# Optimization experiments

Hardware: AMD Instinct MI355X
Metric: run time of the kernel (lower is better)

Reference implementation:

```python
import jax, jax.numpy as jnp
import numpy as np

B, T, C = 64, 256, 1024
H, DH = 16, 64           # n_heads, head_dim (C == H*DH)
NP, WS = 16, 2           # n_patches per side, window_size (T == NP*NP)
EPS = 1e-5


def setup_inputs() -> dict:
    key = jax.random.key(0)
    ks = jax.random.split(key, 8)
    s = lambda k, shape, fan: jax.random.normal(k, shape, jnp.float32) * (fan ** -0.5)
    return dict(
        x=jax.random.normal(ks[0], (B, T, C), jnp.float32),
        ln1_g=jnp.ones((C,), jnp.float32), ln1_b=jnp.zeros((C,), jnp.float32),
        Wq=s(ks[1], (H, C, DH), C), Wk=s(ks[2], (H, C, DH), C), Wv=s(ks[3], (H, C, DH), C),
        Wp=s(ks[4], (C, C), C), bp=jnp.zeros((C,), jnp.float32),
        ln2_g=jnp.ones((C,), jnp.float32), ln2_b=jnp.zeros((C,), jnp.float32),
        W1=s(ks[5], (C, C), C), b1=jnp.zeros((C,), jnp.float32),
        W2=s(ks[6], (C, C), C), b2=jnp.zeros((C,), jnp.float32))


def _ln(x, g, b):
    m = x.mean(-1, keepdims=True)
    v = x.var(-1, keepdims=True)
    return (x - m) * jax.lax.rsqrt(v + EPS) * g + b


def reference(x, ln1_g, ln1_b, Wq, Wk, Wv, Wp, bp, ln2_g, ln2_b, W1, b1, W2, b2):
    h = NP // WS                      # windows per side = 8
    nw = h * h                        # 64 windows of WS*WS = 4 tokens
    xn = _ln(x, ln1_g, ln1_b)
    # window partition: [B, T, C] -> [B*nw, WS*WS, C]
    xw = (xn.reshape(B, h, WS, h, WS, C)
            .transpose(0, 1, 3, 2, 4, 5)
            .reshape(B * nw, WS * WS, C))
    # all-heads batched QKV (original loops over heads; math identical since
    # torch.cat of per-head outputs == head-axis stack then reshape)
    q = jnp.einsum('ntc,hcd->nhtd', xw, Wq)
    k = jnp.einsum('ntc,hcd->nhtd', xw, Wk)
    v = jnp.einsum('ntc,hcd->nhtd', xw, Wv)
    # NOTE: scale is C**-0.5 with C = d_model (faithful to source, not head_dim)
    wei = jax.nn.softmax(jnp.einsum('nhqd,nhkd->nhqk', q, k) * (C ** -0.5), axis=-1)
    att = jnp.einsum('nhqk,nhkd->nhqd', wei, v)
    att = att.transpose(0, 2, 1, 3).reshape(B * nw, WS * WS, C)
    att = att @ Wp + bp
    # residual adds the LayerNorm-ed, window-partitioned x (faithful quirk)
    xr = xw + att
    # reverse window partition -> [B, T, C]
    xr = (xr.reshape(B, h, h, WS, WS, C)
            .transpose(0, 1, 3, 2, 4, 5)
            .reshape(B, T, C))
    ff = jax.nn.gelu(_ln(xr, ln2_g, ln2_b) @ W1 + b1, approximate=False) @ W2 + b2
    return xr + ff
```

## Files before the change

kernel.cpp:

```cpp
#include <hip/hip_runtime.h>
#include <math.h>

typedef unsigned short u16;
typedef unsigned int   u32;

using f32x4  = __attribute__((ext_vector_type(4))) float;
using s16x8  = __attribute__((ext_vector_type(8))) short;
using u16x8  = __attribute__((ext_vector_type(8))) unsigned short;

__device__ __forceinline__ u16 f2b(float f) {
    u32 u = __float_as_uint(f);
    u += 0x7FFFu + ((u >> 16) & 1u);
    return (u16)(u >> 16);
}
__device__ __forceinline__ float b2f(u16 u) { return __uint_as_float(((u32)u) << 16); }

__device__ __forceinline__ int natrow(int R) {
    int b = R >> 8, r8 = R & 255, w = r8 >> 2, t = r8 & 3;
    return (b << 8) + ((((w >> 3) << 1) + (t >> 1)) << 4) + ((w & 7) << 1) + (t & 1);
}

__device__ __forceinline__ void gll16(const void* g, void* l) {
    __builtin_amdgcn_global_load_lds(
        (const __attribute__((address_space(1))) void*)g,
        (__attribute__((address_space(3))) void*)l, 16, 0, 0);
}

__global__ __launch_bounds__(256) void prologue_kernel(
    const float* __restrict__ x, const float* __restrict__ ln1g, const float* __restrict__ ln1b,
    const float* __restrict__ Wq, const float* __restrict__ Wk, const float* __restrict__ Wv,
    const float* __restrict__ Wp, const float* __restrict__ W1, const float* __restrict__ W2,
    u16* __restrict__ WqkvT, u16* __restrict__ WpT, u16* __restrict__ xw_b)
{
    const int bid = blockIdx.x;
    const int tid = threadIdx.x;
    if (bid < 6144) {
        __shared__ float tile[32][33];
        const float* in; u16* out; int Rr, Cc, bx, by;
        if (bid < 3072) {
            const int z = bid >> 6, r = bid & 63;
            bx = r & 1; by = r >> 1;
            in  = (z < 16 ? Wq : z < 32 ? Wk : Wv) + (size_t)(z & 15) * 65536;
            const int h = z & 15, sec = z < 16 ? 0 : (z < 32 ? 1 : 2);
            out = WqkvT + ((size_t)h * 192 + sec * 64) * 1024;
            Rr = 1024; Cc = 64;
        } else {
            const int t = bid - 3072, z = t >> 10, r = t & 1023;
            bx = r & 31; by = r >> 5;
            in  = z == 0 ? Wp : z == 1 ? W1 : W2;
            out = WpT + (size_t)z * 1048576;
            Rr = 1024; Cc = 1024;
        }
        const int tx = tid & 31, ty = tid >> 5;
        const int c  = bx * 32 + tx;
        const int r0 = by * 32;
#pragma unroll
        for (int i = 0; i < 32; i += 8) tile[ty + i][tx] = in[(size_t)(r0 + ty + i) * Cc + c];
        __syncthreads();
        const int orow0 = bx * 32;
        const int ocol  = r0 + tx;
#pragma unroll
        for (int i = 0; i < 32; i += 8)
            out[(size_t)(orow0 + ty + i) * Rr + ocol] = f2b(tile[tx][ty + i]);
    } else {
        __shared__ float red[8];
        const int R   = bid - 6144;
        const int src = natrow(R);
        const float4 v = ((const float4*)(x + (size_t)src * 1024))[tid];
        float s  = v.x + v.y + v.z + v.w;
        float s2 = v.x * v.x + v.y * v.y + v.z * v.z + v.w * v.w;
#pragma unroll
        for (int o = 32; o; o >>= 1) { s += __shfl_xor(s, o); s2 += __shfl_xor(s2, o); }
        const int w = tid >> 6, l = tid & 63;
        if (l == 0) { red[w] = s; red[w + 4] = s2; }
        __syncthreads();
        s  = red[0] + red[1] + red[2] + red[3];
        s2 = red[4] + red[5] + red[6] + red[7];
        const float mean = s * (1.f / 1024.f);
        const float var  = s2 * (1.f / 1024.f) - mean * mean;
        const float rinv = rsqrtf(var + 1e-5f);
        const float4 gv = ((const float4*)ln1g)[tid];
        const float4 bv = ((const float4*)ln1b)[tid];
        ((ushort4*)(xw_b + (size_t)R * 1024))[tid] = make_ushort4(
            f2b((v.x - mean) * rinv * gv.x + bv.x), f2b((v.y - mean) * rinv * gv.y + bv.y),
            f2b((v.z - mean) * rinv * gv.z + bv.z), f2b((v.w - mean) * rinv * gv.w + bv.w));
    }
}

__global__ __launch_bounds__(256) void ln2_kernel(
    const u16* __restrict__ X, const float* __restrict__ g, const float* __restrict__ bta,
    u16* __restrict__ outB)
{
    const int R = blockIdx.x;
    const ushort4 r = ((const ushort4*)(X + (size_t)R * 1024))[threadIdx.x];
    const float x0 = b2f(r.x), x1 = b2f(r.y), x2 = b2f(r.z), x3 = b2f(r.w);
    float s  = x0 + x1 + x2 + x3;
    float s2 = x0 * x0 + x1 * x1 + x2 * x2 + x3 * x3;
#pragma unroll
    for (int o = 32; o; o >>= 1) { s += __shfl_xor(s, o); s2 += __shfl_xor(s2, o); }
    __shared__ float red[8];
    const int w = threadIdx.x >> 6, l = threadIdx.x & 63;
    if (l == 0) { red[w] = s; red[w + 4] = s2; }
    __syncthreads();
    s  = red[0] + red[1] + red[2] + red[3];
    s2 = red[4] + red[5] + red[6] + red[7];
    const float mean = s * (1.f / 1024.f);
    const float var  = s2 * (1.f / 1024.f) - mean * mean;
    const float rinv = rsqrtf(var + 1e-5f);
    const float4 gv = ((const float4*)g)[threadIdx.x];
    const float4 bv = ((const float4*)bta)[threadIdx.x];
    ((ushort4*)(outB + (size_t)R * 1024))[threadIdx.x] = make_ushort4(
        f2b((x0 - mean) * rinv * gv.x + bv.x), f2b((x1 - mean) * rinv * gv.y + bv.y),
        f2b((x2 - mean) * rinv * gv.z + bv.z), f2b((x3 - mean) * rinv * gv.w + bv.w));
}

__global__ __launch_bounds__(512, 2) void gemm_qkv_attn(
    const u16* __restrict__ A, const u16* __restrict__ Bt,
    u16* __restrict__ Att, int M, int K)
{
    extern __shared__ char lds[];
    const int NT = K >> 6;
    const int x = blockIdx.x & 7, i = blockIdx.x >> 3;
    const int sc = i >> 4, u = i & 15;
    const int scr = sc >> 2, scc = sc & 3;
    const int mb = x * 8 + scr * 4 + (u >> 2);
    const int nb = scc * 4 + (u & 3);
    const int row0 = mb * 256, col0 = nb * 192;
    const int tid = threadIdx.x;
    const int w = tid >> 6, l = tid & 63;
    const int wr = w & 3, wcg = w >> 2;
    const int lr = l & 15, kg = l >> 4;
    const int xs = (lr & 7) << 4;
    const int koff[2] = { (kg * 16) ^ xs, (64 + kg * 16) ^ xs };
    const int abase_l = wr * 8192 + lr * 128;
    const int bbase_l = wcg * 12288 + lr * 128;

    f32x4 acc[4][6] = {};
    s16x8 a[4][2], b[6][2];

    auto stageQ = [&](int ts) {
        if (ts >= NT) return;
        const int d = ts & 1, gcolb = ts * 64;
        const int sl = (tid & 7) ^ ((tid >> 3) & 7);
#pragma unroll
        for (int h2 = 0; h2 < 2; ++h2)
#pragma unroll
            for (int j = 0; j < 2; ++j) {
                const int c = j * 512 + tid;
                const int s2 = (c & 7) ^ ((c >> 3) & 7);
                gll16(A + (size_t)(row0 + h2 * 128 + (c >> 3)) * K + gcolb + s2 * 8,
                      lds + d * 32768 + h2 * 16384 + (j * 8 + w) * 1024);
            }
#pragma unroll
        for (int k2 = 0; k2 < 3; ++k2)
            gll16(Bt + (size_t)(col0 + k2 * 64 + (tid >> 3)) * K + gcolb + sl * 8,
                  lds + 65536 + d * 24576 + k2 * 8192 + w * 1024);
    };

#define SB __builtin_amdgcn_sched_barrier(0)
#define WLq(NS) do { asm volatile("s_waitcnt lgkmcnt(" NS ")" ::: "memory"); SB; } while (0)

    stageQ(0);

    for (int t = 0; t < NT; ++t) {
        const char* Ab = lds + (t & 1) * 32768 + abase_l;
        const char* Bb = lds + 65536 + (t & 1) * 24576 + bbase_l;
        asm volatile("s_waitcnt vmcnt(0)" ::: "memory");
        __builtin_amdgcn_s_barrier(); SB;
#pragma unroll
        for (int i2 = 0; i2 < 4; ++i2) a[i2][0] = *(const s16x8*)(Ab + i2 * 2048 + koff[0]);
#pragma unroll
        for (int n = 0; n < 6; ++n)   b[n][0]  = *(const s16x8*)(Bb + n * 2048 + koff[0]);
        SB;
#pragma unroll
        for (int i2 = 0; i2 < 4; ++i2) a[i2][1] = *(const s16x8*)(Ab + i2 * 2048 + koff[1]);
#pragma unroll
        for (int n = 0; n < 6; ++n)   b[n][1]  = *(const s16x8*)(Bb + n * 2048 + koff[1]);
        SB;
        stageQ(t + 1); SB;
        __builtin_amdgcn_s_setprio(1);
        WLq("10");
#pragma unroll
        for (int i2 = 0; i2 < 4; ++i2)
#pragma unroll
            for (int n = 0; n < 6; ++n)
                acc[i2][n] = __builtin_amdgcn_mfma_f32_16x16x32_bf16(a[i2][0], b[n][0], acc[i2][n], 0, 0, 0);
        SB;
        WLq("0");
#pragma unroll
        for (int i2 = 0; i2 < 4; ++i2)
#pragma unroll
            for (int n = 0; n < 6; ++n)
                acc[i2][n] = __builtin_amdgcn_mfma_f32_16x16x32_bf16(a[i2][1], b[n][1], acc[i2][n], 0, 0, 0);
        __builtin_amdgcn_s_setprio(0); SB;
    }
#undef WLq

    __builtin_amdgcn_s_barrier();
    u16* attL = (u16*)lds;
#pragma unroll
    for (int i2 = 0; i2 < 4; ++i2)
#pragma unroll
        for (int n = 0; n < 6; ++n)
#pragma unroll
            for (int j = 0; j < 4; ++j)
                attL[(wr * 64 + i2 * 16 + kg * 4 + j) * 200 + wcg * 96 + n * 16 + lr] =
                    f2b(acc[i2][n][j]);
    __builtin_amdgcn_s_barrier();

    {
        const int wl = tid >> 3, j = tid & 7;
        const float scale = 0.03125f;
        u16x8 qv[4], kv[4], vv[4];
#pragma unroll
        for (int t = 0; t < 4; ++t) {
            qv[t] = *(const u16x8*)&attL[(wl * 4 + t) * 200 + j * 8];
            kv[t] = *(const u16x8*)&attL[(wl * 4 + t) * 200 + 64 + j * 8];
            vv[t] = *(const u16x8*)&attL[(wl * 4 + t) * 200 + 128 + j * 8];
        }
        float qf[4][8], kf[4][8];
#pragma unroll
        for (int t = 0; t < 4; ++t)
#pragma unroll
            for (int c = 0; c < 8; ++c) { qf[t][c] = b2f(qv[t][c]); kf[t][c] = b2f(kv[t][c]); }
        float s[4][4];
#pragma unroll
        for (int t = 0; t < 4; ++t)
#pragma unroll
            for (int u2 = 0; u2 < 4; ++u2) {
                float p = qf[t][0] * kf[u2][0];
#pragma unroll
                for (int c = 1; c < 8; ++c) p += qf[t][c] * kf[u2][c];
                p += __shfl_xor(p, 1); p += __shfl_xor(p, 2); p += __shfl_xor(p, 4);
                s[t][u2] = p * scale;
            }
#pragma unroll
        for (int t = 0; t < 4; ++t) {
            const float m = fmaxf(fmaxf(s[t][0], s[t][1]), fmaxf(s[t][2], s[t][3]));
            const float e0 = expf(s[t][0] - m), e1 = expf(s[t][1] - m);
            const float e2 = expf(s[t][2] - m), e3 = expf(s[t][3] - m);
            const float inv = 1.f / (e0 + e1 + e2 + e3);
            u16x8 o;
#pragma unroll
            for (int c = 0; c < 8; ++c)
                o[c] = f2b((e0 * b2f(vv[0][c]) + e1 * b2f(vv[1][c]) +
                            e2 * b2f(vv[2][c]) + e3 * b2f(vv[3][c])) * inv);
            *(u16x8*)(Att + (size_t)(row0 + wl * 4 + t) * 1024 + nb * 64 + j * 8) = o;
        }
    }
#undef SB
}

template<int MODE>
__global__ __launch_bounds__(512, 2) void gemm256(
    const u16* __restrict__ A, const u16* __restrict__ Bt,
    const float* __restrict__ bias, const void* __restrict__ resid,
    void* __restrict__ Out, int M, int N, int K, int LDA, int NB)
{
    extern __shared__ char lds[];
    const int NT = K >> 6;
    const int nblk = gridDim.x;
    const int x = blockIdx.x & 7, i = blockIdx.x >> 3;
    const int R = (nblk >> 3) / NB;
    const int ncs = NB >> 2;
    const int sc = i >> 4, u = i & 15;
    const int scr = sc / ncs, scc = sc - scr * ncs;
    const int mb = x * R + scr * 4 + (u >> 2);
    const int nb = scc * 4 + (u & 3);
    const int row0 = mb * 256, col0 = nb * 256;
    const int tid = threadIdx.x;
    const int w = tid >> 6, l = tid & 63;
    const int wr = w >> 2, wc = w & 3;
    const int lr = l & 15, kg = l >> 4;
    const int xs = (lr & 7) << 4;
    const int koff[2] = { (kg * 16) ^ xs, (64 + kg * 16) ^ xs };
    const int abase_l = wr * 8192 + lr * 128;
    const int bbase_l = wc * 4096 + lr * 128;

    f32x4 acc[2][2][4][2] = {};
    s16x8 a0[4][2], a1[4][2], b0[2][2], b1[2][2];

    auto stage = [&](int ts, int item) {
        if (ts >= NT) return;
        const int d = ts & 1;
        const int isB = item & 1, h = item >> 1;
        char* lbase = lds + (isB ? 65536 : 0) + d * 32768 + h * 16384;
        const u16* gptr = isB ? Bt : A;
        const int ld = isB ? K : LDA;
        const int blk0 = (isB ? col0 : row0) + h * 128;
#pragma unroll
        for (int j = 0; j < 2; ++j) {
            const int p = j * 512 + tid;
            const int q = p ^ ((p >> 3) & 7);
            gll16(gptr + (size_t)(blk0 + (q >> 3)) * ld + ts * 64 + (q & 7) * 8,
                  lbase + (j * 8 + w) * 1024);
        }
    };

#define SB __builtin_amdgcn_sched_barrier(0)
#define LOAD_A(dst, qm) do { \
    _Pragma("unroll") for (int kk = 0; kk < 2; ++kk) \
    _Pragma("unroll") for (int i2 = 0; i2 < 4; ++i2) \
        dst[i2][kk] = *(const s16x8*)(Ab + (qm) * 16384 + abase_l + i2 * 2048 + koff[kk]); \
} while (0)
#define LOAD_B(dst, qn) do { \
    _Pragma("unroll") for (int kk = 0; kk < 2; ++kk) \
    _Pragma("unroll") for (int n = 0; n < 2; ++n) \
        dst[n][kk] = *(const s16x8*)(Bb + (qn) * 16384 + bbase_l + n * 2048 + koff[kk]); \
} while (0)
#define LGKM0 do { asm volatile("s_waitcnt lgkmcnt(0)" ::: "memory"); SB; } while (0)
#define MFMA_Q(qm, qn, aa, bb) do { \
    __builtin_amdgcn_s_setprio(1); \
    _Pragma("unroll") for (int kk = 0; kk < 2; ++kk) \
    _Pragma("unroll") for (int i2 = 0; i2 < 4; ++i2) \
    _Pragma("unroll") for (int n = 0; n < 2; ++n) \
        acc[qm][qn][i2][n] = __builtin_amdgcn_mfma_f32_16x16x32_bf16( \
            aa[i2][kk], bb[n][kk], acc[qm][qn][i2][n], 0, 0, 0); \
    __builtin_amdgcn_s_setprio(0); SB; \
} while (0)
#define GATE(NSTR) do { \
    asm volatile("s_waitcnt vmcnt(" NSTR ")" ::: "memory"); \
    __builtin_amdgcn_s_barrier(); SB; \
} while (0)

    stage(0, 0); stage(0, 1); stage(0, 2); stage(0, 3);

    for (int t = 0; t < NT - 1; ++t) {
        const char* Ab = lds + (t & 1) * 32768;
        const char* Bb = lds + 65536 + (t & 1) * 32768;
        GATE("4");
        LOAD_A(a0, 0); LOAD_B(b0, 0); SB;
        stage(t + 1, 0); SB;
        LGKM0;
        MFMA_Q(0, 0, a0, b0);
        GATE("4");
        LOAD_A(a1, 1); SB;
        stage(t + 1, 1); SB;
        LGKM0;
        MFMA_Q(1, 0, a1, b0);
        GATE("4");
        LOAD_B(b1, 1); SB;
        stage(t + 1, 2); SB;
        LGKM0;
        MFMA_Q(1, 1, a1, b1);
        stage(t + 1, 3); SB;
        MFMA_Q(0, 1, a0, b1);
    }
    {
        const int t = NT - 1;
        const char* Ab = lds + (t & 1) * 32768;
        const char* Bb = lds + 65536 + (t & 1) * 32768;
        GATE("4");
        LOAD_A(a0, 0); LOAD_B(b0, 0); SB;
        LGKM0;
        MFMA_Q(0, 0, a0, b0);
        GATE("2");
        LOAD_A(a1, 1); SB;
        LGKM0;
        MFMA_Q(1, 0, a1, b0);
        GATE("0");
        LOAD_B(b1, 1); SB;
        LGKM0;
        MFMA_Q(1, 1, a1, b1);
        MFMA_Q(0, 1, a0, b1);
    }
#undef SB
#undef LOAD_A
#undef LOAD_B
#undef LGKM0
#undef MFMA_Q
#undef GATE

#pragma unroll
    for (int qm = 0; qm < 2; ++qm)
#pragma unroll
    for (int i2 = 0; i2 < 4; ++i2) {
        const int grb = row0 + qm * 128 + wr * 64 + i2 * 16 + kg * 4;
#pragma unroll
        for (int qn = 0; qn < 2; ++qn)
#pragma unroll
        for (int n = 0; n < 2; ++n) {
            const int gc = col0 + qn * 128 + wc * 32 + n * 16 + lr;
#pragma unroll
            for (int j = 0; j < 4; ++j) {
                const int gr = grb + j;
                const float v = acc[qm][qn][i2][n][j];
                if (MODE == 2) {
                    const float tt = v + bias[gc];
                    ((u16*)Out)[(size_t)gr * N + gc] = f2b(0.5f * tt * (1.f + erff(tt * 0.70710678118f)));
                } else if (MODE == 3) {
                    ((float*)Out)[(size_t)natrow(gr) * N + gc] =
                        v + bias[gc] + b2f(((const u16*)resid)[(size_t)gr * N + gc]);
                } else {
                    ((u16*)Out)[(size_t)gr * N + gc] =
                        f2b(v + bias[gc] + b2f(((const u16*)resid)[(size_t)gr * N + gc]));
                }
            }
        }
    }
}

extern "C" void kernel_launch(void* const* d_in, const int* in_sizes, int n_in,
                              void* d_out, int out_size, void* d_ws, size_t ws_size,
                              hipStream_t stream)
{
    const float* x    = (const float*)d_in[0];
    const float* ln1g = (const float*)d_in[1];
    const float* ln1b = (const float*)d_in[2];
    const float* Wq   = (const float*)d_in[3];
    const float* Wk   = (const float*)d_in[4];
    const float* Wv   = (const float*)d_in[5];
    const float* Wp   = (const float*)d_in[6];
    const float* bp   = (const float*)d_in[7];
    const float* ln2g = (const float*)d_in[8];
    const float* ln2b = (const float*)d_in[9];
    const float* W1   = (const float*)d_in[10];
    const float* b1   = (const float*)d_in[11];
    const float* W2   = (const float*)d_in[12];
    const float* b2   = (const float*)d_in[13];
    float* out = (float*)d_out;

    char* ws = (char*)d_ws;
    const size_t MB = 1024 * 1024;
    u16* xr_b  = (u16*)ws;
    u16* xw_b  = (u16*)(ws + 32 * MB);
    u16* att   = (u16*)(ws + 64 * MB);
    u16* h1b   = (u16*)(ws + 96 * MB);
    u16* ln2bf = (u16*)(ws + 128 * MB);
    u16* WqkvT = (u16*)(ws + 192 * MB);
    u16* WpT   = (u16*)(ws + 198 * MB);
    u16* W1T   = WpT + (1u << 20);
    u16* W2T   = W1T + (1u << 20);

    (void)hipFuncSetAttribute((const void*)gemm_qkv_attn, hipFuncAttributeMaxDynamicSharedMemorySize, 114688);
    (void)hipFuncSetAttribute((const void*)gemm256<2>, hipFuncAttributeMaxDynamicSharedMemorySize, 131072);
    (void)hipFuncSetAttribute((const void*)gemm256<3>, hipFuncAttributeMaxDynamicSharedMemorySize, 131072);
    (void)hipFuncSetAttribute((const void*)gemm256<5>, hipFuncAttributeMaxDynamicSharedMemorySize, 131072);

    const int M = 16384, K = 1024;

    prologue_kernel<<<22528, 256, 0, stream>>>(x, ln1g, ln1b, Wq, Wk, Wv,
                                               Wp, W1, W2, WqkvT, WpT, xw_b);

    gemm_qkv_attn<<<1024, 512, 114688, stream>>>(xw_b, WqkvT, att, M, K);

    gemm256<5><<<256, 512, 131072, stream>>>(att, WpT, bp, xw_b, xr_b, M, 1024, K, K, 4);

    ln2_kernel<<<16384, 256, 0, stream>>>(xr_b, ln2g, ln2b, ln2bf);

    gemm256<2><<<256, 512, 131072, stream>>>(ln2bf, W1T, b1, nullptr, h1b, M, 1024, K, K, 4);

    gemm256<3><<<256, 512, 131072, stream>>>(h1b, W2T, b2, xr_b, out, M, 1024, K, K, 4);
}
```

Measured before the change: 285.6 us.

## Fold LN2 into W1 GEMM via row stats from projection epilogue

Removes the standalone LN2 kernel and its bf16 normalized buffer. The projection GEMM epilogue now accumulates per-row sum and sum-of-squares with atomics. The FC1 GEMM reads the un-normalized residual and applies the mean/rstd correction in its epilogue, with gamma folded into W1 and precomputed column vectors (gamma·W1, beta·W1+b1) built in the prologue. This adds a memset, atomics and some precision risk from the E[x^2]-mean^2 variance and the bf16 rounding of gamma-scaled weights.

Measured after the change: 304.5 us. 1.07x slower.

```diff
diff --git a/kernel.cpp b/kernel.cpp
--- a/kernel.cpp
+++ b/kernel.cpp
@@ -30,39 +30,44 @@
     const float* __restrict__ x, const float* __restrict__ ln1g, const float* __restrict__ ln1b,
     const float* __restrict__ Wq, const float* __restrict__ Wk, const float* __restrict__ Wv,
     const float* __restrict__ Wp, const float* __restrict__ W1, const float* __restrict__ W2,
-    u16* __restrict__ WqkvT, u16* __restrict__ WpT, u16* __restrict__ xw_b)
+    const float* __restrict__ ln2g, const float* __restrict__ ln2b, const float* __restrict__ b1,
+    u16* __restrict__ WqkvT, u16* __restrict__ WpT, u16* __restrict__ xw_b,
+    float* __restrict__ cvec, float* __restrict__ dvp)
 {
     const int bid = blockIdx.x;
     const int tid = threadIdx.x;
     if (bid < 6144) {
         __shared__ float tile[32][33];
-        const float* in; u16* out; int Rr, Cc, bx, by;
+        const float* in; u16* out; int Cc, bx, by, gfold = 0;
         if (bid < 3072) {
             const int z = bid >> 6, r = bid & 63;
             bx = r & 1; by = r >> 1;
             in  = (z < 16 ? Wq : z < 32 ? Wk : Wv) + (size_t)(z & 15) * 65536;
             const int h = z & 15, sec = z < 16 ? 0 : (z < 32 ? 1 : 2);
             out = WqkvT + ((size_t)h * 192 + sec * 64) * 1024;
-            Rr = 1024; Cc = 64;
+            Cc = 64;
         } else {
             const int t = bid - 3072, z = t >> 10, r = t & 1023;
             bx = r & 31; by = r >> 5;
             in  = z == 0 ? Wp : z == 1 ? W1 : W2;
             out = WpT + (size_t)z * 1048576;
-            Rr = 1024; Cc = 1024;
+            Cc = 1024; gfold = (z == 1);
         }
         const int tx = tid & 31, ty = tid >> 5;
         const int c  = bx * 32 + tx;
         const int r0 = by * 32;
 #pragma unroll
-        for (int i = 0; i < 32; i += 8) tile[ty + i][tx] = in[(size_t)(r0 + ty + i) * Cc + c];
+        for (int i = 0; i < 32; i += 8) {
+            const float gs = gfold ? ln2g[r0 + ty + i] : 1.f;
+            tile[ty + i][tx] = in[(size_t)(r0 + ty + i) * Cc + c] * gs;
+        }
         __syncthreads();
         const int orow0 = bx * 32;
         const int ocol  = r0 + tx;
 #pragma unroll
         for (int i = 0; i < 32; i += 8)
-            out[(size_t)(orow0 + ty + i) * Rr + ocol] = f2b(tile[tx][ty + i]);
-    } else {
+            out[(size_t)(orow0 + ty + i) * 1024 + ocol] = f2b(tile[tx][ty + i]);
+    } else if (bid < 22528) {
         __shared__ float red[8];
         const int R   = bid - 6144;
         const int src = natrow(R);
@@ -84,34 +89,27 @@
         ((ushort4*)(xw_b + (size_t)R * 1024))[tid] = make_ushort4(
             f2b((v.x - mean) * rinv * gv.x + bv.x), f2b((v.y - mean) * rinv * gv.y + bv.y),
             f2b((v.z - mean) * rinv * gv.z + bv.z), f2b((v.w - mean) * rinv * gv.w + bv.w));
+    } else {
+        const int kb = bid - 22528;
+        const int n0 = tid * 4;
+        float pc[4] = {0, 0, 0, 0}, pd[4] = {0, 0, 0, 0};
+        for (int r = 0; r < 16; ++r) {
+            const int k = kb * 16 + r;
+            const float gk = ln2g[k], bk = ln2b[k];
+            const float4 wv = *(const float4*)&W1[(size_t)k * 1024 + n0];
+            pc[0] += gk * wv.x; pc[1] += gk * wv.y; pc[2] += gk * wv.z; pc[3] += gk * wv.w;
+            pd[0] += bk * wv.x; pd[1] += bk * wv.y; pd[2] += bk * wv.z; pd[3] += bk * wv.w;
+        }
+        if (kb == 0) {
+            const float4 bb = *(const float4*)&b1[n0];
+            pd[0] += bb.x; pd[1] += bb.y; pd[2] += bb.z; pd[3] += bb.w;
+        }
+#pragma unroll
+        for (int c = 0; c < 4; ++c) {
+            atomicAdd(&cvec[n0 + c], pc[c]);
+            atomicAdd(&dvp[n0 + c], pd[c]);
+        }
     }
-}
-
-__global__ __launch_bounds__(256) void ln2_kernel(
-    const u16* __restrict__ X, const float* __restrict__ g, const float* __restrict__ bta,
-    u16* __restrict__ outB)
-{
-    const int R = blockIdx.x;
-    const ushort4 r = ((const ushort4*)(X + (size_t)R * 1024))[threadIdx.x];
-    const float x0 = b2f(r.x), x1 = b2f(r.y), x2 = b2f(r.z), x3 = b2f(r.w);
-    float s  = x0 + x1 + x2 + x3;
-    float s2 = x0 * x0 + x1 * x1 + x2 * x2 + x3 * x3;
-#pragma unroll
-    for (int o = 32; o; o >>= 1) { s += __shfl_xor(s, o); s2 += __shfl_xor(s2, o); }
-    __shared__ float red[8];
-    const int w = threadIdx.x >> 6, l = threadIdx.x & 63;
-    if (l == 0) { red[w] = s; red[w + 4] = s2; }
-    __syncthreads();
-    s  = red[0] + red[1] + red[2] + red[3];
-    s2 = red[4] + red[5] + red[6] + red[7];
-    const float mean = s * (1.f / 1024.f);
-    const float var  = s2 * (1.f / 1024.f) - mean * mean;
-    const float rinv = rsqrtf(var + 1e-5f);
-    const float4 gv = ((const float4*)g)[threadIdx.x];
-    const float4 bv = ((const float4*)bta)[threadIdx.x];
-    ((ushort4*)(outB + (size_t)R * 1024))[threadIdx.x] = make_ushort4(
-        f2b((x0 - mean) * rinv * gv.x + bv.x), f2b((x1 - mean) * rinv * gv.y + bv.y),
-        f2b((x2 - mean) * rinv * gv.z + bv.z), f2b((x3 - mean) * rinv * gv.w + bv.w));
 }
 
 __global__ __launch_bounds__(512, 2) void gemm_qkv_attn(
@@ -255,7 +253,9 @@
 __global__ __launch_bounds__(512, 2) void gemm256(
     const u16* __restrict__ A, const u16* __restrict__ Bt,
     const float* __restrict__ bias, const void* __restrict__ resid,
-    void* __restrict__ Out, int M, int N, int K, int LDA, int NB)
+    void* __restrict__ Out, float* __restrict__ stats,
+    const float* __restrict__ cvec, const float* __restrict__ dvp,
+    int M, int N, int K, int LDA, int NB)
 {
     extern __shared__ char lds[];
     const int NT = K >> 6;
@@ -278,7 +278,7 @@
     const int bbase_l = wc * 4096 + lr * 128;
 
     f32x4 acc[2][2][4][2] = {};
-    s16x8 a0[4][2], a1[4][2], b0[2][2], b1[2][2];
+    s16x8 a0[4][2], a1[4][2], b0[2][2], b1r[2][2];
 
     auto stage = [&](int ts, int item) {
         if (ts >= NT) return;
@@ -339,12 +339,12 @@
         LGKM0;
         MFMA_Q(1, 0, a1, b0);
         GATE("4");
-        LOAD_B(b1, 1); SB;
+        LOAD_B(b1r, 1); SB;
         stage(t + 1, 2); SB;
         LGKM0;
-        MFMA_Q(1, 1, a1, b1);
+        MFMA_Q(1, 1, a1, b1r);
         stage(t + 1, 3); SB;
-        MFMA_Q(0, 1, a0, b1);
+        MFMA_Q(0, 1, a0, b1r);
     }
     {
         const int t = NT - 1;
@@ -359,10 +359,10 @@
         LGKM0;
         MFMA_Q(1, 0, a1, b0);
         GATE("0");
-        LOAD_B(b1, 1); SB;
+        LOAD_B(b1r, 1); SB;
         LGKM0;
-        MFMA_Q(1, 1, a1, b1);
-        MFMA_Q(0, 1, a0, b1);
+        MFMA_Q(1, 1, a1, b1r);
+        MFMA_Q(0, 1, a0, b1r);
     }
 #undef SB
 #undef LOAD_A
@@ -371,30 +371,72 @@
 #undef MFMA_Q
 #undef GATE
 
-#pragma unroll
-    for (int qm = 0; qm < 2; ++qm)
-#pragma unroll
-    for (int i2 = 0; i2 < 4; ++i2) {
-        const int grb = row0 + qm * 128 + wr * 64 + i2 * 16 + kg * 4;
-#pragma unroll
-        for (int qn = 0; qn < 2; ++qn)
-#pragma unroll
-        for (int n = 0; n < 2; ++n) {
-            const int gc = col0 + qn * 128 + wc * 32 + n * 16 + lr;
-#pragma unroll
-            for (int j = 0; j < 4; ++j) {
-                const int gr = grb + j;
-                const float v = acc[qm][qn][i2][n][j];
-                if (MODE == 2) {
-                    const float tt = v + bias[gc];
-                    ((u16*)Out)[(size_t)gr * N + gc] = f2b(0.5f * tt * (1.f + erff(tt * 0.70710678118f)));
-                } else if (MODE == 3) {
+    if (MODE == 3) {
+#pragma unroll
+        for (int qm = 0; qm < 2; ++qm)
+#pragma unroll
+        for (int i2 = 0; i2 < 4; ++i2) {
+            const int grb = row0 + qm * 128 + wr * 64 + i2 * 16 + kg * 4;
+#pragma unroll
+            for (int qn = 0; qn < 2; ++qn)
+#pragma unroll
+            for (int n = 0; n < 2; ++n) {
+                const int gc = col0 + qn * 128 + wc * 32 + n * 16 + lr;
+#pragma unroll
+                for (int j = 0; j < 4; ++j) {
+                    const int gr = grb + j;
                     ((float*)Out)[(size_t)natrow(gr) * N + gc] =
-                        v + bias[gc] + b2f(((const u16*)resid)[(size_t)gr * N + gc]);
-                } else {
-                    ((u16*)Out)[(size_t)gr * N + gc] =
-                        f2b(v + bias[gc] + b2f(((const u16*)resid)[(size_t)gr * N + gc]));
+                        acc[qm][qn][i2][n][j] + bias[gc] + b2f(((const u16*)resid)[(size_t)gr * N + gc]);
                 }
+            }
+        }
+    } else if (MODE == 6) {
+#pragma unroll
+        for (int qm = 0; qm < 2; ++qm)
+#pragma unroll
+        for (int i2 = 0; i2 < 4; ++i2)
+#pragma unroll
+        for (int j = 0; j < 4; ++j) {
+            const int gr = row0 + qm * 128 + wr * 64 + i2 * 16 + kg * 4 + j;
+            float s1 = 0.f, s2 = 0.f;
+#pragma unroll
+            for (int qn = 0; qn < 2; ++qn)
+#pragma unroll
+            for (int n = 0; n < 2; ++n) {
+                const int gc = col0 + qn * 128 + wc * 32 + n * 16 + lr;
+                const float rs = acc[qm][qn][i2][n][j] + bias[gc] +
+                                 b2f(((const u16*)resid)[(size_t)gr * N + gc]);
+                ((u16*)Out)[(size_t)gr * N + gc] = f2b(rs);
+                s1 += rs; s2 += rs * rs;
+            }
+#pragma unroll
+            for (int o = 1; o < 16; o <<= 1) { s1 += __shfl_xor(s1, o); s2 += __shfl_xor(s2, o); }
+            if (lr == 0) {
+                atomicAdd(&stats[gr * 2],     s1);
+                atomicAdd(&stats[gr * 2 + 1], s2);
+            }
+        }
+    } else {
+#pragma unroll
+        for (int qm = 0; qm < 2; ++qm)
+#pragma unroll
+        for (int i2 = 0; i2 < 4; ++i2)
+#pragma unroll
+        for (int j = 0; j < 4; ++j) {
+            const int gr = row0 + qm * 128 + wr * 64 + i2 * 16 + kg * 4 + j;
+            const float sm  = stats[gr * 2], sq = stats[gr * 2 + 1];
+            const float mu  = sm * (1.f / 1024.f);
+            const float var = sq * (1.f / 1024.f) - mu * mu;
+            const float ri  = rsqrtf(var + 1e-5f);
+            const float rim = -ri * mu;
+#pragma unroll
+            for (int qn = 0; qn < 2; ++qn)
+#pragma unroll
+            for (int n = 0; n < 2; ++n) {
+                const int gc = col0 + qn * 128 + wc * 32 + n * 16 + lr;
+                const float tt = ri * acc[qm][qn][i2][n][j] + rim * cvec[gc] + dvp[gc];
+                ((u16*)Out)[(size_t)gr * N + gc] =
+                    f2b(0.5f * tt * (1.f + erff(tt * 0.70710678118f)));
             }
         }
     }
@@ -422,33 +464,39 @@
 
     char* ws = (char*)d_ws;
     const size_t MB = 1024 * 1024;
-    u16* xr_b  = (u16*)ws;
-    u16* xw_b  = (u16*)(ws + 32 * MB);
-    u16* att   = (u16*)(ws + 64 * MB);
-    u16* h1b   = (u16*)(ws + 96 * MB);
-    u16* ln2bf = (u16*)(ws + 128 * MB);
-    u16* WqkvT = (u16*)(ws + 192 * MB);
-    u16* WpT   = (u16*)(ws + 198 * MB);
-    u16* W1T   = WpT + (1u << 20);
-    u16* W2T   = W1T + (1u << 20);
+    u16*   xr_b  = (u16*)ws;
+    u16*   xw_b  = (u16*)(ws + 32 * MB);
+    u16*   att   = (u16*)(ws + 64 * MB);
+    u16*   h1b   = (u16*)(ws + 96 * MB);
+    float* stats = (float*)(ws + 128 * MB);
+    float* cvec  = (float*)(ws + 128 * MB + 131072);
+    float* dvp   = (float*)(ws + 128 * MB + 135168);
+    u16*   WqkvT = (u16*)(ws + 192 * MB);
+    u16*   WpT   = (u16*)(ws + 198 * MB);
+    u16*   W1T   = WpT + (1u << 20);
+    u16*   W2T   = W1T + (1u << 20);
 
     (void)hipFuncSetAttribute((const void*)gemm_qkv_attn, hipFuncAttributeMaxDynamicSharedMemorySize, 114688);
-    (void)hipFuncSetAttribute((const void*)gemm256<2>, hipFuncAttributeMaxDynamicSharedMemorySize, 131072);
     (void)hipFuncSetAttribute((const void*)gemm256<3>, hipFuncAttributeMaxDynamicSharedMemorySize, 131072);
-    (void)hipFuncSetAttribute((const void*)gemm256<5>, hipFuncAttributeMaxDynamicSharedMemorySize, 131072);
+    (void)hipFuncSetAttribute((const void*)gemm256<6>, hipFuncAttributeMaxDynamicSharedMemorySize, 131072);
+    (void)hipFuncSetAttribute((const void*)gemm256<7>, hipFuncAttributeMaxDynamicSharedMemorySize, 131072);
 
     const int M = 16384, K = 1024;
 
-    prologue_kernel<<<22528, 256, 0, stream>>>(x, ln1g, ln1b, Wq, Wk, Wv,
-                                               Wp, W1, W2, WqkvT, WpT, xw_b);
+    (void)hipMemsetAsync(ws + 128 * MB, 0, 139264, stream);
+
+    prologue_kernel<<<22592, 256, 0, stream>>>(x, ln1g, ln1b, Wq, Wk, Wv,
+                                               Wp, W1, W2, ln2g, ln2b, b1,
+                                               WqkvT, WpT, xw_b, cvec, dvp);
 
     gemm_qkv_attn<<<1024, 512, 114688, stream>>>(xw_b, WqkvT, att, M, K);
 
-    gemm256<5><<<256, 512, 131072, stream>>>(att, WpT, bp, xw_b, xr_b, M, 1024, K, K, 4);
-
-    ln2_kernel<<<16384, 256, 0, stream>>>(xr_b, ln2g, ln2b, ln2bf);
-
-    gemm256<2><<<256, 512, 131072, stream>>>(ln2bf, W1T, b1, nullptr, h1b, M, 1024, K, K, 4);
-
-    gemm256<3><<<256, 512, 131072, stream>>>(h1b, W2T, b2, xr_b, out, M, 1024, K, K, 4);
-}
+    gemm256<6><<<256, 512, 131072, stream>>>(att, WpT, bp, xw_b, xr_b,
+                                             stats, nullptr, nullptr, M, 1024, K, K, 4);
+
+    gemm256<7><<<256, 512, 131072, stream>>>(xr_b, W1T, nullptr, nullptr, h1b,
+                                             stats, cvec, dvp, M, 1024, K, K, 4);
+
+    gemm256<3><<<256, 512, 131072, stream>>>(h1b, W2T, b2, xr_b, out,
+                                             nullptr, nullptr, nullptr, M, 1024, K, K, 4);
+}
```

## Deepen GEMM prefetch to two tiles ahead with barrier-interleaved MFMA phases

Applied to the files above, without the earlier changes.

Both the QKV/attention GEMM and the generic tiled GEMM now issue global-to-LDS loads two K-tiles ahead instead of one. Each tile's work is split into phases, and LDS fragment reads, partial staging into the buffer just consumed, and MFMA groups are interleaved with explicit barriers. In the QKV kernel the B fragments are now split into two halves of three columns, which lowers register pressure. The goal is to hide more global-load latency behind MFMA work. The cost is that many more workgroup barriers are added per K step, and reusing the same LDS buffer for tile t+2 depends on the register reads finishing before the barrier.

Measured after the change: 302.5 us. 1.06x slower.

```diff
diff --git a/kernel.cpp b/kernel.cpp
--- a/kernel.cpp
+++ b/kernel.cpp
@@ -136,21 +136,23 @@
     const int bbase_l = wcg * 12288 + lr * 128;
 
     f32x4 acc[4][6] = {};
-    s16x8 a[4][2], b[6][2];
-
-    auto stageQ = [&](int ts) {
+    s16x8 a[4][2], bA[3], bB[3];
+
+    auto stageA = [&](int ts, int h2) {
+        if (ts >= NT) return;
+        const int d = ts & 1, gcolb = ts * 64;
+#pragma unroll
+        for (int j = 0; j < 2; ++j) {
+            const int c = j * 512 + tid;
+            const int s2 = (c & 7) ^ ((c >> 3) & 7);
+            gll16(A + (size_t)(row0 + h2 * 128 + (c >> 3)) * K + gcolb + s2 * 8,
+                  lds + d * 32768 + h2 * 16384 + (j * 8 + w) * 1024);
+        }
+    };
+    auto stageB = [&](int ts) {
         if (ts >= NT) return;
         const int d = ts & 1, gcolb = ts * 64;
         const int sl = (tid & 7) ^ ((tid >> 3) & 7);
-#pragma unroll
-        for (int h2 = 0; h2 < 2; ++h2)
-#pragma unroll
-            for (int j = 0; j < 2; ++j) {
-                const int c = j * 512 + tid;
-                const int s2 = (c & 7) ^ ((c >> 3) & 7);
-                gll16(A + (size_t)(row0 + h2 * 128 + (c >> 3)) * K + gcolb + s2 * 8,
-                      lds + d * 32768 + h2 * 16384 + (j * 8 + w) * 1024);
-            }
 #pragma unroll
         for (int k2 = 0; k2 < 3; ++k2)
             gll16(Bt + (size_t)(col0 + k2 * 64 + (tid >> 3)) * K + gcolb + sl * 8,
@@ -158,43 +160,65 @@
     };
 
 #define SB __builtin_amdgcn_sched_barrier(0)
-#define WLq(NS) do { asm volatile("s_waitcnt lgkmcnt(" NS ")" ::: "memory"); SB; } while (0)
-
-    stageQ(0);
-
-    for (int t = 0; t < NT; ++t) {
+#define BARR do { __builtin_amdgcn_s_barrier(); SB; } while (0)
+#define LGKM0 do { asm volatile("s_waitcnt lgkmcnt(0)" ::: "memory"); SB; } while (0)
+#define RA do { _Pragma("unroll") for (int i2 = 0; i2 < 4; ++i2) { \
+    a[i2][0] = *(const s16x8*)(Ab + i2 * 2048 + koff[0]); \
+    a[i2][1] = *(const s16x8*)(Ab + i2 * 2048 + koff[1]); } } while (0)
+#define RB(dst, kk, nlo) do { _Pragma("unroll") for (int n = 0; n < 3; ++n) \
+    dst[n] = *(const s16x8*)(Bb + ((nlo) + n) * 2048 + koff[kk]); } while (0)
+#define M12(kk, bb, nlo) do { \
+    __builtin_amdgcn_s_setprio(1); \
+    _Pragma("unroll") for (int i2 = 0; i2 < 4; ++i2) \
+    _Pragma("unroll") for (int n = 0; n < 3; ++n) \
+        acc[i2][(nlo) + n] = __builtin_amdgcn_mfma_f32_16x16x32_bf16( \
+            a[i2][kk], bb[n], acc[i2][(nlo) + n], 0, 0, 0); \
+    __builtin_amdgcn_s_setprio(0); SB; } while (0)
+
+    stageA(0, 0); stageA(0, 1); stageB(0); stageA(1, 0); stageA(1, 1);
+    asm volatile("s_waitcnt vmcnt(4)" ::: "memory");
+    __builtin_amdgcn_s_barrier();
+
+    for (int t = 0; t < NT - 1; ++t) {
+        const char* Ab = lds + (t & 1) * 32768 + abase_l;
+        const char* Bb = lds + 65536 + (t & 1) * 24576 + bbase_l;
+        RA; RB(bA, 0, 0); SB;
+        stageB(t + 1); SB;
+        BARR; LGKM0;
+        M12(0, bA, 0);
+        BARR;
+        RB(bB, 0, 3); SB;
+        stageA(t + 2, 0); SB;
+        BARR; LGKM0;
+        M12(0, bB, 3);
+        BARR;
+        RB(bA, 1, 0); SB;
+        stageA(t + 2, 1); SB;
+        BARR; LGKM0;
+        M12(1, bA, 0);
+        BARR;
+        RB(bB, 1, 3); SB;
+        BARR; LGKM0;
+        M12(1, bB, 3);
+        asm volatile("s_waitcnt vmcnt(4)" ::: "memory"); SB;
+        BARR;
+    }
+    {
+        const int t = NT - 1;
         const char* Ab = lds + (t & 1) * 32768 + abase_l;
         const char* Bb = lds + 65536 + (t & 1) * 24576 + bbase_l;
         asm volatile("s_waitcnt vmcnt(0)" ::: "memory");
         __builtin_amdgcn_s_barrier(); SB;
-#pragma unroll
-        for (int i2 = 0; i2 < 4; ++i2) a[i2][0] = *(const s16x8*)(Ab + i2 * 2048 + koff[0]);
-#pragma unroll
-        for (int n = 0; n < 6; ++n)   b[n][0]  = *(const s16x8*)(Bb + n * 2048 + koff[0]);
-        SB;
-#pragma unroll
-        for (int i2 = 0; i2 < 4; ++i2) a[i2][1] = *(const s16x8*)(Ab + i2 * 2048 + koff[1]);
-#pragma unroll
-        for (int n = 0; n < 6; ++n)   b[n][1]  = *(const s16x8*)(Bb + n * 2048 + koff[1]);
-        SB;
-        stageQ(t + 1); SB;
-        __builtin_amdgcn_s_setprio(1);
-        WLq("10");
-#pragma unroll
-        for (int i2 = 0; i2 < 4; ++i2)
-#pragma unroll
-            for (int n = 0; n < 6; ++n)
-                acc[i2][n] = __builtin_amdgcn_mfma_f32_16x16x32_bf16(a[i2][0], b[n][0], acc[i2][n], 0, 0, 0);
-        SB;
-        WLq("0");
-#pragma unroll
-        for (int i2 = 0; i2 < 4; ++i2)
-#pragma unroll
-            for (int n = 0; n < 6; ++n)
-                acc[i2][n] = __builtin_amdgcn_mfma_f32_16x16x32_bf16(a[i2][1], b[n][1], acc[i2][n], 0, 0, 0);
-        __builtin_amdgcn_s_setprio(0); SB;
-    }
-#undef WLq
+        RA; RB(bA, 0, 0); SB; LGKM0; M12(0, bA, 0);
+        RB(bB, 0, 3); SB; LGKM0; M12(0, bB, 3);
+        RB(bA, 1, 0); SB; LGKM0; M12(1, bA, 0);
+        RB(bB, 1, 3); SB; LGKM0; M12(1, bB, 3);
+    }
+#undef RA
+#undef RB
+#undef M12
+#undef BARR
+#undef LGKM0
 
     __builtin_amdgcn_s_barrier();
     u16* attL = (u16*)lds;
@@ -298,6 +322,8 @@
     };
 
 #define SB __builtin_amdgcn_sched_barrier(0)
+#define BARR do { __builtin_amdgcn_s_barrier(); SB; } while (0)
+#define LGKM0 do { asm volatile("s_waitcnt lgkmcnt(0)" ::: "memory"); SB; } while (0)
 #define LOAD_A(dst, qm) do { \
     _Pragma("unroll") for (int kk = 0; kk < 2; ++kk) \
     _Pragma("unroll") for (int i2 = 0; i2 < 4; ++i2) \
@@ -308,7 +334,6 @@
     _Pragma("unroll") for (int n = 0; n < 2; ++n) \
         dst[n][kk] = *(const s16x8*)(Bb + (qn) * 16384 + bbase_l + n * 2048 + koff[kk]); \
 } while (0)
-#define LGKM0 do { asm volatile("s_waitcnt lgkmcnt(0)" ::: "memory"); SB; } while (0)
 #define MFMA_Q(qm, qn, aa, bb) do { \
     __builtin_amdgcn_s_setprio(1); \
     _Pragma("unroll") for (int kk = 0; kk < 2; ++kk) \
@@ -318,58 +343,52 @@
             aa[i2][kk], bb[n][kk], acc[qm][qn][i2][n], 0, 0, 0); \
     __builtin_amdgcn_s_setprio(0); SB; \
 } while (0)
-#define GATE(NSTR) do { \
-    asm volatile("s_waitcnt vmcnt(" NSTR ")" ::: "memory"); \
-    __builtin_amdgcn_s_barrier(); SB; \
-} while (0)
 
     stage(0, 0); stage(0, 1); stage(0, 2); stage(0, 3);
+    stage(1, 0); stage(1, 1); stage(1, 2); stage(1, 3);
+    asm volatile("s_waitcnt vmcnt(8)" ::: "memory");
+    __builtin_amdgcn_s_barrier();
 
     for (int t = 0; t < NT - 1; ++t) {
         const char* Ab = lds + (t & 1) * 32768;
         const char* Bb = lds + 65536 + (t & 1) * 32768;
-        GATE("4");
         LOAD_A(a0, 0); LOAD_B(b0, 0); SB;
-        stage(t + 1, 0); SB;
-        LGKM0;
+        BARR; LGKM0;
         MFMA_Q(0, 0, a0, b0);
-        GATE("4");
+        BARR;
         LOAD_A(a1, 1); SB;
-        stage(t + 1, 1); SB;
-        LGKM0;
+        stage(t + 2, 0); SB;
+        BARR; LGKM0;
         MFMA_Q(1, 0, a1, b0);
-        GATE("4");
+        BARR;
         LOAD_B(b1, 1); SB;
-        stage(t + 1, 2); SB;
-        LGKM0;
+        stage(t + 2, 1); stage(t + 2, 2); SB;
+        BARR; LGKM0;
         MFMA_Q(1, 1, a1, b1);
-        stage(t + 1, 3); SB;
+        BARR;
+        stage(t + 2, 3); SB;
+        BARR;
         MFMA_Q(0, 1, a0, b1);
+        asm volatile("s_waitcnt vmcnt(8)" ::: "memory"); SB;
+        BARR;
     }
     {
         const int t = NT - 1;
         const char* Ab = lds + (t & 1) * 32768;
         const char* Bb = lds + 65536 + (t & 1) * 32768;
-        GATE("4");
-        LOAD_A(a0, 0); LOAD_B(b0, 0); SB;
-        LGKM0;
-        MFMA_Q(0, 0, a0, b0);
-        GATE("2");
-        LOAD_A(a1, 1); SB;
-        LGKM0;
-        MFMA_Q(1, 0, a1, b0);
-        GATE("0");
-        LOAD_B(b1, 1); SB;
-        LGKM0;
-        MFMA_Q(1, 1, a1, b1);
+        asm volatile("s_waitcnt vmcnt(0)" ::: "memory");
+        __builtin_amdgcn_s_barrier(); SB;
+        LOAD_A(a0, 0); LOAD_B(b0, 0); SB; LGKM0; MFMA_Q(0, 0, a0, b0);
+        LOAD_A(a1, 1); SB; LGKM0; MFMA_Q(1, 0, a1, b0);
+        LOAD_B(b1, 1); SB; LGKM0; MFMA_Q(1, 1, a1, b1);
         MFMA_Q(0, 1, a0, b1);
     }
 #undef SB
+#undef BARR
+#undef LGKM0
 #undef LOAD_A
 #undef LOAD_B
-#undef LGKM0
 #undef MFMA_Q
-#undef GATE
 
 #pragma unroll
     for (int qm = 0; qm < 2; ++qm)
```
